# Kernel optimization log

Measured on AMD Instinct MI355X. Metric: run time of the kernel, lower is better.

## Reference

```python
import jax, jax.numpy as jnp
import numpy as np

N_NODES = 50000
N_EDGES = 800000
N_POS = 200000
N_NEG = 200000
D_IN = 128
D_OUT = 128
NEG_SLOPE = 0.2  # DGL GATConv default leaky_relu slope


def setup_inputs() -> dict:
    key = jax.random.key(0)
    ks = jax.random.split(key, 12)
    inp = {
        "x": jax.random.normal(ks[0], (N_NODES, D_IN), dtype=jnp.float32),
        "W": jax.random.normal(ks[1], (D_IN, D_OUT), dtype=jnp.float32) / np.sqrt(D_IN),
        "attn_l": jax.random.normal(ks[2], (D_OUT,), dtype=jnp.float32) / np.sqrt(D_OUT),
        "attn_r": jax.random.normal(ks[3], (D_OUT,), dtype=jnp.float32) / np.sqrt(D_OUT),
        "bias": jnp.zeros((D_OUT,), dtype=jnp.float32),
        "src": jax.random.randint(ks[4], (N_EDGES,), 0, N_NODES, dtype=jnp.int32),
        "dst": jax.random.randint(ks[5], (N_EDGES,), 0, N_NODES, dtype=jnp.int32),
        "pos_src": jax.random.randint(ks[6], (N_POS,), 0, N_NODES, dtype=jnp.int32),
        "pos_dst": jax.random.randint(ks[7], (N_POS,), 0, N_NODES, dtype=jnp.int32),
        "neg_src": jax.random.randint(ks[8], (N_NEG,), 0, N_NODES, dtype=jnp.int32),
        "neg_dst": jax.random.randint(ks[9], (N_NEG,), 0, N_NODES, dtype=jnp.int32),
    }
    return inp


def _gat_conv(x, W, attn_l, attn_r, bias, src, dst):
    # DGL GATConv, num_heads=1, feat_drop=0, activation=relu
    feat = x @ W                               # [N, D_OUT]
    el = feat @ attn_l                         # [N]
    er = feat @ attn_r                         # [N]
    e = jax.nn.leaky_relu(el[src] + er[dst], NEG_SLOPE)  # [E]
    # edge softmax grouped by destination node
    m = jax.ops.segment_max(e, dst, num_segments=N_NODES)   # [N]
    ee = jnp.exp(e - m[dst])
    s = jax.ops.segment_sum(ee, dst, num_segments=N_NODES)  # [N]
    a = ee / s[dst]                            # [E]
    # weighted message aggregation
    h = jax.ops.segment_sum(a[:, None] * feat[src], dst, num_segments=N_NODES)
    return jax.nn.relu(h + bias)               # [N, D_OUT]


def reference(x, W, attn_l, attn_r, bias, src, dst, pos_src, pos_dst, neg_src, neg_dst):
    h = _gat_conv(x, W, attn_l, attn_r, bias, src, dst)
    # ScorePredictor: u_dot_v on each scoring graph -> [E, 1]
    pos_score = jnp.sum(h[pos_src] * h[pos_dst], axis=-1, keepdims=True)
    neg_score = jnp.sum(h[neg_src] * h[neg_dst], axis=-1, keepdims=True)
    return (pos_score, neg_score)
```

## Files before the change

kernel.cpp:

```cpp
#include <hip/hip_runtime.h>
#include <hip/hip_bf16.h>
#include <cstdint>
#include <cstddef>

#define N_NODES 50000
#define N_EDGES 800000
#define N_POS   200000
#define N_NEG   200000
#define DIM     128
#define NEG_SLOPE 0.2f

#define BUCK_SHIFT 7
#define BUCK_NODES 128
#define NBUCK 391
#define SLABCAP 2560
#define BIN_CHUNK 4096
#define NB_BIN 196

#define SUB_NODES 32
#define SUBCAP 704

typedef _Float16 half8 __attribute__((ext_vector_type(8)));

__global__ __launch_bounds__(256) void gemm_feat(
    const float* __restrict__ x, const float* __restrict__ W,
    const float* __restrict__ attn_l, const float* __restrict__ attn_r,
    half8* __restrict__ feat16, float* __restrict__ el, float* __restrict__ er,
    int n)
{
  __shared__ float xs[64][33];
  __shared__ float ws[32][128];
  const int tid = threadIdx.x;
  const int row0 = blockIdx.x * 64;
  const int rg = tid & 15;
  const int cg = tid >> 4;

  float acc[4][8];
#pragma unroll
  for (int i = 0; i < 4; ++i)
#pragma unroll
    for (int j = 0; j < 8; ++j) acc[i][j] = 0.f;

  for (int kc = 0; kc < DIM; kc += 32) {
    {
      const int r = tid >> 2;
      const int c = (tid & 3) * 8;
      const int grow = row0 + r;
      float4 v0 = make_float4(0.f, 0.f, 0.f, 0.f);
      float4 v1 = make_float4(0.f, 0.f, 0.f, 0.f);
      if (grow < n) {
        const float* srcp = &x[(size_t)grow * DIM + kc + c];
        v0 = *(const float4*)(srcp);
        v1 = *(const float4*)(srcp + 4);
      }
      xs[r][c + 0] = v0.x; xs[r][c + 1] = v0.y; xs[r][c + 2] = v0.z; xs[r][c + 3] = v0.w;
      xs[r][c + 4] = v1.x; xs[r][c + 5] = v1.y; xs[r][c + 6] = v1.z; xs[r][c + 7] = v1.w;
    }
    {
      const int r = tid >> 3;
      const int c = (tid & 7) * 16;
      const float* srcp = &W[(size_t)(kc + r) * DIM + c];
      *(float4*)&ws[r][c + 0]  = *(const float4*)(srcp + 0);
      *(float4*)&ws[r][c + 4]  = *(const float4*)(srcp + 4);
      *(float4*)&ws[r][c + 8]  = *(const float4*)(srcp + 8);
      *(float4*)&ws[r][c + 12] = *(const float4*)(srcp + 12);
    }
    __syncthreads();
#pragma unroll 8
    for (int k = 0; k < 32; ++k) {
      const float a0 = xs[rg * 4 + 0][k];
      const float a1 = xs[rg * 4 + 1][k];
      const float a2 = xs[rg * 4 + 2][k];
      const float a3 = xs[rg * 4 + 3][k];
      const float4 w0 = *(const float4*)&ws[k][cg * 8];
      const float4 w1 = *(const float4*)&ws[k][cg * 8 + 4];
      const float wv[8] = {w0.x, w0.y, w0.z, w0.w, w1.x, w1.y, w1.z, w1.w};
#pragma unroll
      for (int j = 0; j < 8; ++j) {
        acc[0][j] = fmaf(a0, wv[j], acc[0][j]);
        acc[1][j] = fmaf(a1, wv[j], acc[1][j]);
        acc[2][j] = fmaf(a2, wv[j], acc[2][j]);
        acc[3][j] = fmaf(a3, wv[j], acc[3][j]);
      }
    }
    __syncthreads();
  }

#pragma unroll
  for (int i = 0; i < 4; ++i) {
    const int grow = row0 + rg * 4 + i;
    if (grow < n) {
      half8 o;
#pragma unroll
      for (int j = 0; j < 8; ++j) o[j] = (_Float16)acc[i][j];
      feat16[(size_t)grow * 16 + cg] = o;
    }
  }

  const float4 al0 = *(const float4*)&attn_l[cg * 8];
  const float4 al1 = *(const float4*)&attn_l[cg * 8 + 4];
  const float4 ar0 = *(const float4*)&attn_r[cg * 8];
  const float4 ar1 = *(const float4*)&attn_r[cg * 8 + 4];
  const float alv[8] = {al0.x, al0.y, al0.z, al0.w, al1.x, al1.y, al1.z, al1.w};
  const float arv[8] = {ar0.x, ar0.y, ar0.z, ar0.w, ar1.x, ar1.y, ar1.z, ar1.w};
  float* redl = &ws[0][0];
  float* redr = redl + 64 * 17;
#pragma unroll
  for (int i = 0; i < 4; ++i) {
    float pl = 0.f, pr = 0.f;
#pragma unroll
    for (int j = 0; j < 8; ++j) {
      pl = fmaf(acc[i][j], alv[j], pl);
      pr = fmaf(acc[i][j], arv[j], pr);
    }
    redl[(rg * 4 + i) * 17 + cg] = pl;
    redr[(rg * 4 + i) * 17 + cg] = pr;
  }
  __syncthreads();
  if (tid < 64) {
    const int grow = row0 + tid;
    if (grow < n) {
      float sl = 0.f, sr = 0.f;
#pragma unroll
      for (int c = 0; c < 16; ++c) {
        sl += redl[tid * 17 + c];
        sr += redr[tid * 17 + c];
      }
      el[grow] = sl;
      er[grow] = sr;
    }
  }
}

__global__ __launch_bounds__(256) void bin_kernel(
    const int* __restrict__ src, const int* __restrict__ dst,
    unsigned int* __restrict__ slab, int* __restrict__ slab_cursor)
{
  __shared__ int hist[NBUCK];
  __shared__ int base_s[NBUCK];
  __shared__ int cur[NBUCK];
  const int tid = threadIdx.x;
  const int e0 = blockIdx.x * BIN_CHUNK;
  for (int i = tid; i < NBUCK; i += 256) { hist[i] = 0; cur[i] = 0; }
  __syncthreads();
  for (int i = tid; i < BIN_CHUNK; i += 256) {
    const int e = e0 + i;
    if (e < N_EDGES) atomicAdd(&hist[dst[e] >> BUCK_SHIFT], 1);
  }
  __syncthreads();
  for (int i = tid; i < NBUCK; i += 256) {
    const int h = hist[i];
    base_s[i] = h ? atomicAdd(&slab_cursor[i], h) : 0;
  }
  __syncthreads();
  for (int i = tid; i < BIN_CHUNK; i += 256) {
    const int e = e0 + i;
    if (e >= N_EDGES) continue;
    const int d = dst[e];
    const int bk = d >> BUCK_SHIFT;
    const int p = atomicAdd(&cur[bk], 1);
    int idx = base_s[bk] + p;
    if (idx >= SLABCAP) idx = SLABCAP - 1;
    slab[(size_t)bk * SLABCAP + idx] =
        ((unsigned int)src[e] << BUCK_SHIFT) | (unsigned int)(d & (BUCK_NODES - 1));
  }
}

__global__ __launch_bounds__(256) void aggregate_kernel(
    const half8* __restrict__ feat16, const float* __restrict__ el,
    const float* __restrict__ er,
    const unsigned int* __restrict__ slab, const int* __restrict__ slab_cursor,
    const float* __restrict__ bias, half8* __restrict__ h16)
{
  __shared__ unsigned int csr[SUBCAP];
  __shared__ float wbuf[SUBCAP];
  __shared__ int cnt_l[SUB_NODES];
  __shared__ int start_l[SUB_NODES];
  __shared__ int cur_l[SUB_NODES];
  const int b = blockIdx.x >> 2;
  const int sub = blockIdx.x & 3;
  const int tid = threadIdx.x;
  const int cnt = min(slab_cursor[b], SLABCAP);
  const unsigned int* sb = slab + (size_t)b * SLABCAP;
  const int node0 = (b << BUCK_SHIFT) + sub * SUB_NODES;

  if (tid < SUB_NODES) cnt_l[tid] = 0;
  __syncthreads();
  for (int i = tid; i < cnt; i += 256) {
    const int d = sb[i] & (BUCK_NODES - 1);
    if ((d >> 5) == sub) atomicAdd(&cnt_l[d & 31], 1);
  }
  __syncthreads();
  if (tid < 64) {
    const int v = (tid < SUB_NODES) ? cnt_l[tid] : 0;
    int inc = v;
#pragma unroll
    for (int d = 1; d < 32; d <<= 1) {
      const int t = __shfl_up(inc, d, 64);
      if (tid >= d) inc += t;
    }
    if (tid < SUB_NODES) { start_l[tid] = inc - v; cur_l[tid] = 0; }
  }
  __syncthreads();
  for (int i = tid; i < cnt; i += 256) {
    const unsigned int r = sb[i];
    const int d = r & (BUCK_NODES - 1);
    if ((d >> 5) == sub) {
      const int p = atomicAdd(&cur_l[d & 31], 1);
      const int idx = start_l[d & 31] + p;
      if (idx < SUBCAP) csr[idx] = r;
    }
  }
  __syncthreads();

  const int lane = tid & 63;
  const int ql = lane & 15;
  const int qid = (tid >> 6) * 4 + (lane >> 4);
  const float4 b0 = *(const float4*)&bias[ql * 8];
  const float4 b1 = *(const float4*)&bias[ql * 8 + 4];
  const float bb[8] = {b0.x, b0.y, b0.z, b0.w, b1.x, b1.y, b1.z, b1.w};

  for (int nl = qid; nl < SUB_NODES; nl += 16) {
    const int node = node0 + nl;
    if (node >= N_NODES) break;
    const int beg = start_l[nl];
    const int cnum = cnt_l[nl];
    const float ern = er[node];

    float m = -INFINITY;
    for (int c = ql; c < cnum; c += 16) {
      const unsigned int r = csr[beg + c];
      const float v = el[r >> BUCK_SHIFT] + ern;
      const float e = (v > 0.f) ? v : NEG_SLOPE * v;
      wbuf[beg + c] = e;
      m = fmaxf(m, e);
    }
#pragma unroll
    for (int o = 1; o < 16; o <<= 1) m = fmaxf(m, __shfl_xor(m, o, 64));

    float sp = 0.f;
    for (int c = ql; c < cnum; c += 16) {
      const float w = __expf(wbuf[beg + c] - m);
      wbuf[beg + c] = w;
      sp += w;
    }
#pragma unroll
    for (int o = 1; o < 16; o <<= 1) sp += __shfl_xor(sp, o, 64);

    float acc[8];
#pragma unroll
    for (int k = 0; k < 8; ++k) acc[k] = 0.f;
    int t = 0;
    for (; t + 4 <= cnum; t += 4) {
      const float w0 = wbuf[beg + t + 0];
      const float w1 = wbuf[beg + t + 1];
      const float w2 = wbuf[beg + t + 2];
      const float w3 = wbuf[beg + t + 3];
      const int s0 = (int)(csr[beg + t + 0] >> BUCK_SHIFT);
      const int s1 = (int)(csr[beg + t + 1] >> BUCK_SHIFT);
      const int s2 = (int)(csr[beg + t + 2] >> BUCK_SHIFT);
      const int s3 = (int)(csr[beg + t + 3] >> BUCK_SHIFT);
      const half8 f0 = feat16[(size_t)s0 * 16 + ql];
      const half8 f1 = feat16[(size_t)s1 * 16 + ql];
      const half8 f2 = feat16[(size_t)s2 * 16 + ql];
      const half8 f3 = feat16[(size_t)s3 * 16 + ql];
#pragma unroll
      for (int k = 0; k < 8; ++k) {
        acc[k] = fmaf(w0, (float)f0[k], acc[k]);
        acc[k] = fmaf(w1, (float)f1[k], acc[k]);
        acc[k] = fmaf(w2, (float)f2[k], acc[k]);
        acc[k] = fmaf(w3, (float)f3[k], acc[k]);
      }
    }
    for (; t < cnum; ++t) {
      const float w = wbuf[beg + t];
      const int sid = (int)(csr[beg + t] >> BUCK_SHIFT);
      const half8 f = feat16[(size_t)sid * 16 + ql];
#pragma unroll
      for (int k = 0; k < 8; ++k) acc[k] = fmaf(w, (float)f[k], acc[k]);
    }

    const float inv = (cnum > 0) ? 1.f / sp : 0.f;
    half8 o;
#pragma unroll
    for (int k = 0; k < 8; ++k)
      o[k] = (_Float16)fmaxf(acc[k] * inv + bb[k], 0.f);
    h16[(size_t)node * 16 + ql] = o;
  }
}

__global__ __launch_bounds__(256) void score_kernel(
    const half8* __restrict__ h16,
    const int* __restrict__ pos_src, const int* __restrict__ pos_dst,
    const int* __restrict__ neg_src, const int* __restrict__ neg_dst,
    float* __restrict__ out, int ntot)
{
  const int wid = (int)((blockIdx.x * blockDim.x + threadIdx.x) >> 6);
  const int lane = threadIdx.x & 63;
  const int q = lane >> 4;
  const int ql = lane & 15;
  const int p = wid * 4 + q;
  int a = 0, b = 0;
  if (p < N_POS)      { a = pos_src[p]; b = pos_dst[p]; }
  else if (p < ntot)  { a = neg_src[p - N_POS]; b = neg_dst[p - N_POS]; }
  const half8 ha = h16[(size_t)a * 16 + ql];
  const half8 hb = h16[(size_t)b * 16 + ql];
  float sum = 0.f;
#pragma unroll
  for (int k = 0; k < 8; ++k) sum = fmaf((float)ha[k], (float)hb[k], sum);
#pragma unroll
  for (int o = 8; o > 0; o >>= 1) sum += __shfl_xor(sum, o, 64);
  if (ql == 0 && p < ntot) out[p] = sum;
}

extern "C" void kernel_launch(void* const* d_in, const int* in_sizes, int n_in,
                              void* d_out, int out_size, void* d_ws, size_t ws_size,
                              hipStream_t stream) {
  const float* x      = (const float*)d_in[0];
  const float* W      = (const float*)d_in[1];
  const float* attn_l = (const float*)d_in[2];
  const float* attn_r = (const float*)d_in[3];
  const float* bias   = (const float*)d_in[4];
  const int* src      = (const int*)d_in[5];
  const int* dst      = (const int*)d_in[6];
  const int* pos_src  = (const int*)d_in[7];
  const int* pos_dst  = (const int*)d_in[8];
  const int* neg_src  = (const int*)d_in[9];
  const int* neg_dst  = (const int*)d_in[10];
  float* out = (float*)d_out;

  char* ws = (char*)d_ws;
  const size_t F16B = (size_t)N_NODES * DIM * sizeof(_Float16);
  half8* feat16          = (half8*)(ws);
  half8* h16             = (half8*)(ws + F16B);
  float* el              = (float*)(ws + 2 * F16B);
  float* er              = (float*)(ws + 2 * F16B + 200000);
  int*   slab_cursor     = (int*)  (ws + 2 * F16B + 400000);
  unsigned int* slab     = (unsigned int*)(ws + 2 * F16B + 401664);

  hipMemsetAsync(slab_cursor, 0, NBUCK * sizeof(int), stream);

  gemm_feat<<<(N_NODES + 63) / 64, 256, 0, stream>>>(
      x, W, attn_l, attn_r, feat16, el, er, N_NODES);
  bin_kernel<<<NB_BIN, 256, 0, stream>>>(src, dst, slab, slab_cursor);
  aggregate_kernel<<<NBUCK * 4, 256, 0, stream>>>(
      feat16, el, er, slab, slab_cursor, bias, h16);
  score_kernel<<<((N_POS + N_NEG) / 4 + 3) / 4, 256, 0, stream>>>(
      h16, pos_src, pos_dst, neg_src, neg_dst, out, N_POS + N_NEG);
}
```

Baseline: 207.7 us.

## Split aggregate buckets into 8 sub-blocks, unroll gathers by 8, batch score pairs

The aggregate kernel now splits each 128-node bucket into 8 sub-blocks of 16 nodes instead of 4 of 32. Each quarter-wave handles exactly one node, which doubles the block count. The feature gather loop adds an 8-wide unrolled stage that issues more independent loads in flight. The score kernel makes each 16-lane group process 4 pairs, batching the index and h loads to raise memory-level parallelism. In exchange, every extra sub-block rescans the whole bucket slab, and SUBCAP is tighter, which risks overflow truncation for high-degree nodes.

```diff
diff --git a/kernel.cpp b/kernel.cpp
--- a/kernel.cpp
+++ b/kernel.cpp
@@ -17,8 +17,9 @@
 #define BIN_CHUNK 4096
 #define NB_BIN 196
 
-#define SUB_NODES 32
-#define SUBCAP 704
+#define NSUB 8
+#define SUB_NODES 16
+#define SUBCAP 384
 
 typedef _Float16 half8 __attribute__((ext_vector_type(8)));
 
@@ -177,8 +178,8 @@
   __shared__ int cnt_l[SUB_NODES];
   __shared__ int start_l[SUB_NODES];
   __shared__ int cur_l[SUB_NODES];
-  const int b = blockIdx.x >> 2;
-  const int sub = blockIdx.x & 3;
+  const int b = blockIdx.x >> 3;
+  const int sub = blockIdx.x & 7;
   const int tid = threadIdx.x;
   const int cnt = min(slab_cursor[b], SLABCAP);
   const unsigned int* sb = slab + (size_t)b * SLABCAP;
@@ -188,14 +189,14 @@
   __syncthreads();
   for (int i = tid; i < cnt; i += 256) {
     const int d = sb[i] & (BUCK_NODES - 1);
-    if ((d >> 5) == sub) atomicAdd(&cnt_l[d & 31], 1);
+    if ((d >> 4) == sub) atomicAdd(&cnt_l[d & 15], 1);
   }
   __syncthreads();
   if (tid < 64) {
     const int v = (tid < SUB_NODES) ? cnt_l[tid] : 0;
     int inc = v;
 #pragma unroll
-    for (int d = 1; d < 32; d <<= 1) {
+    for (int d = 1; d < 16; d <<= 1) {
       const int t = __shfl_up(inc, d, 64);
       if (tid >= d) inc += t;
     }
@@ -205,9 +206,9 @@
   for (int i = tid; i < cnt; i += 256) {
     const unsigned int r = sb[i];
     const int d = r & (BUCK_NODES - 1);
-    if ((d >> 5) == sub) {
-      const int p = atomicAdd(&cur_l[d & 31], 1);
-      const int idx = start_l[d & 31] + p;
+    if ((d >> 4) == sub) {
+      const int p = atomicAdd(&cur_l[d & 15], 1);
+      const int idx = start_l[d & 15] + p;
       if (idx < SUBCAP) csr[idx] = r;
     }
   }
@@ -220,9 +221,9 @@
   const float4 b1 = *(const float4*)&bias[ql * 8 + 4];
   const float bb[8] = {b0.x, b0.y, b0.z, b0.w, b1.x, b1.y, b1.z, b1.w};
 
-  for (int nl = qid; nl < SUB_NODES; nl += 16) {
-    const int node = node0 + nl;
-    if (node >= N_NODES) break;
+  const int nl = qid;
+  const int node = node0 + nl;
+  if (node < N_NODES) {
     const int beg = start_l[nl];
     const int cnum = cnt_l[nl];
     const float ern = er[node];
@@ -251,26 +252,33 @@
 #pragma unroll
     for (int k = 0; k < 8; ++k) acc[k] = 0.f;
     int t = 0;
+    for (; t + 8 <= cnum; t += 8) {
+      float wv[8]; int sv[8]; half8 fv[8];
+#pragma unroll
+      for (int u = 0; u < 8; ++u) {
+        wv[u] = wbuf[beg + t + u];
+        sv[u] = (int)(csr[beg + t + u] >> BUCK_SHIFT);
+      }
+#pragma unroll
+      for (int u = 0; u < 8; ++u) fv[u] = feat16[(size_t)sv[u] * 16 + ql];
+#pragma unroll
+      for (int u = 0; u < 8; ++u)
+#pragma unroll
+        for (int k = 0; k < 8; ++k) acc[k] = fmaf(wv[u], (float)fv[u][k], acc[k]);
+    }
     for (; t + 4 <= cnum; t += 4) {
-      const float w0 = wbuf[beg + t + 0];
-      const float w1 = wbuf[beg + t + 1];
-      const float w2 = wbuf[beg + t + 2];
-      const float w3 = wbuf[beg + t + 3];
-      const int s0 = (int)(csr[beg + t + 0] >> BUCK_SHIFT);
-      const int s1 = (int)(csr[beg + t + 1] >> BUCK_SHIFT);
-      const int s2 = (int)(csr[beg + t + 2] >> BUCK_SHIFT);
-      const int s3 = (int)(csr[beg + t + 3] >> BUCK_SHIFT);
-      const half8 f0 = feat16[(size_t)s0 * 16 + ql];
-      const half8 f1 = feat16[(size_t)s1 * 16 + ql];
-      const half8 f2 = feat16[(size_t)s2 * 16 + ql];
-      const half8 f3 = feat16[(size_t)s3 * 16 + ql];
-#pragma unroll
-      for (int k = 0; k < 8; ++k) {
-        acc[k] = fmaf(w0, (float)f0[k], acc[k]);
-        acc[k] = fmaf(w1, (float)f1[k], acc[k]);
-        acc[k] = fmaf(w2, (float)f2[k], acc[k]);
-        acc[k] = fmaf(w3, (float)f3[k], acc[k]);
-      }
+      float wv[4]; int sv[4]; half8 fv[4];
+#pragma unroll
+      for (int u = 0; u < 4; ++u) {
+        wv[u] = wbuf[beg + t + u];
+        sv[u] = (int)(csr[beg + t + u] >> BUCK_SHIFT);
+      }
+#pragma unroll
+      for (int u = 0; u < 4; ++u) fv[u] = feat16[(size_t)sv[u] * 16 + ql];
+#pragma unroll
+      for (int u = 0; u < 4; ++u)
+#pragma unroll
+        for (int k = 0; k < 8; ++k) acc[k] = fmaf(wv[u], (float)fv[u][k], acc[k]);
     }
     for (; t < cnum; ++t) {
       const float w = wbuf[beg + t];
@@ -299,18 +307,40 @@
   const int lane = threadIdx.x & 63;
   const int q = lane >> 4;
   const int ql = lane & 15;
-  const int p = wid * 4 + q;
-  int a = 0, b = 0;
-  if (p < N_POS)      { a = pos_src[p]; b = pos_dst[p]; }
-  else if (p < ntot)  { a = neg_src[p - N_POS]; b = neg_dst[p - N_POS]; }
-  const half8 ha = h16[(size_t)a * 16 + ql];
-  const half8 hb = h16[(size_t)b * 16 + ql];
-  float sum = 0.f;
-#pragma unroll
-  for (int k = 0; k < 8; ++k) sum = fmaf((float)ha[k], (float)hb[k], sum);
-#pragma unroll
-  for (int o = 8; o > 0; o >>= 1) sum += __shfl_xor(sum, o, 64);
-  if (ql == 0 && p < ntot) out[p] = sum;
+  const int base = (wid * 4 + q) * 4;
+
+  int av[4], bv[4];
+#pragma unroll
+  for (int u = 0; u < 4; ++u) {
+    const int p = base + u;
+    int a = 0, b = 0;
+    if (p < N_POS)      { a = pos_src[p]; b = pos_dst[p]; }
+    else if (p < ntot)  { a = neg_src[p - N_POS]; b = neg_dst[p - N_POS]; }
+    av[u] = a; bv[u] = b;
+  }
+  half8 ha[4], hb[4];
+#pragma unroll
+  for (int u = 0; u < 4; ++u) {
+    ha[u] = h16[(size_t)av[u] * 16 + ql];
+    hb[u] = h16[(size_t)bv[u] * 16 + ql];
+  }
+  float sum[4];
+#pragma unroll
+  for (int u = 0; u < 4; ++u) {
+    float s = 0.f;
+#pragma unroll
+    for (int k = 0; k < 8; ++k) s = fmaf((float)ha[u][k], (float)hb[u][k], s);
+#pragma unroll
+    for (int o = 8; o > 0; o >>= 1) s += __shfl_xor(s, o, 64);
+    sum[u] = s;
+  }
+  if (ql == 0) {
+#pragma unroll
+    for (int u = 0; u < 4; ++u) {
+      const int p = base + u;
+      if (p < ntot) out[p] = sum[u];
+    }
+  }
 }
 
 extern "C" void kernel_launch(void* const* d_in, const int* in_sizes, int n_in,
@@ -343,8 +373,8 @@
   gemm_feat<<<(N_NODES + 63) / 64, 256, 0, stream>>>(
       x, W, attn_l, attn_r, feat16, el, er, N_NODES);
   bin_kernel<<<NB_BIN, 256, 0, stream>>>(src, dst, slab, slab_cursor);
-  aggregate_kernel<<<NBUCK * 4, 256, 0, stream>>>(
+  aggregate_kernel<<<NBUCK * NSUB, 256, 0, stream>>>(
       feat16, el, er, slab, slab_cursor, bias, h16);
-  score_kernel<<<((N_POS + N_NEG) / 4 + 3) / 4, 256, 0, stream>>>(
+  score_kernel<<<((N_POS + N_NEG + 15) / 16 + 3) / 4, 256, 0, stream>>>(
       h16, pos_src, pos_dst, neg_src, neg_dst, out, N_POS + N_NEG);
 }
```

Measured after the change: 208.5 us. Within noise of the previous version (+0.4%).
